# Performance work log

Measured on AMD Instinct MI355X. Metric: run time of the kernel, lower is better.

## Reference

```python
import jax, jax.numpy as jnp
import numpy as np

DIM = 768
N_HEADS = 12
HEAD_DIM = DIM // N_HEADS
SCALE = HEAD_DIM ** -0.5


def setup_inputs() -> dict:
    key = jax.random.key(0)
    ks = jax.random.split(key, 5)
    B, N = 8, 1024
    x = jax.random.normal(ks[0], (B, N, DIM), dtype=jnp.float32)
    # Linear weights stored as (in, out) for x @ W; torch stores (out, in).
    w_qkv = jax.random.normal(ks[1], (DIM, 3 * DIM), dtype=jnp.float32) * (DIM ** -0.5)
    b_qkv = jnp.zeros((3 * DIM,), dtype=jnp.float32)
    w_proj = jax.random.normal(ks[2], (DIM, DIM), dtype=jnp.float32) * (DIM ** -0.5)
    b_proj = jnp.zeros((DIM,), dtype=jnp.float32)
    return {"x": x, "w_qkv": w_qkv, "b_qkv": b_qkv, "w_proj": w_proj, "b_proj": b_proj}


def reference(x, w_qkv, b_qkv, w_proj, b_proj):
    B, N, _ = x.shape
    qkv = x @ w_qkv + b_qkv                       # [B, N, 3*dim]
    qkv = qkv.reshape(B, N, 3, N_HEADS, HEAD_DIM)
    qkv = jnp.transpose(qkv, (2, 0, 3, 1, 4))     # [3, B, H, N, hd]
    q, k, v = qkv[0], qkv[1], qkv[2]
    attn = jnp.einsum("bhqd,bhkd->bhqk", q, k) * SCALE
    attn = jax.nn.softmax(attn, axis=-1)
    out = jnp.einsum("bhqk,bhkd->bhqd", attn, v)  # [B, H, N, hd]
    out = jnp.transpose(out, (0, 2, 1, 3)).reshape(B, N, DIM)
    return out @ w_proj + b_proj
```

## Files before the change

### kernel.cpp

```cpp
#include <hip/hip_runtime.h>
#include <cstdint>

#define DIM 768
#define NH 12
#define HD 64
#define SEQ 1024
#define NBH 96

#define QOFF  ((size_t)0)
#define KOFF  ((size_t)6291456)
#define VOFF  ((size_t)12582912)
#define AOFF  ((size_t)18874368)
#define XOFF  ((size_t)25165824)
#define WQOFF ((size_t)31457280)
#define WPOFF ((size_t)33226752)

#define QSCALE 0.18033688f

#define WAIT_VM0   __builtin_amdgcn_s_waitcnt(0x0F70)
#define BAR        __builtin_amdgcn_s_barrier()
#define CFENCE     __asm__ __volatile__("" ::: "memory")

typedef __attribute__((ext_vector_type(8))) __bf16 bf16x8;
typedef __attribute__((ext_vector_type(2))) __bf16 bf16x2;
typedef __attribute__((ext_vector_type(4))) float f32x4;
typedef __attribute__((ext_vector_type(4))) short s16x4;
typedef unsigned short u16;

__device__ __forceinline__ u16 f2bf(float f) {
    union { float f; unsigned u; } x; x.f = f;
    unsigned r = x.u + 0x7fffu + ((x.u >> 16) & 1u);
    return (u16)(r >> 16);
}

__device__ __forceinline__ unsigned pkbf(float a, float b) {
#if __has_builtin(__builtin_amdgcn_cvt_pk_bf16_f32)
    bf16x2 v = __builtin_amdgcn_cvt_pk_bf16_f32(a, b);
    union { bf16x2 v; unsigned u; } c; c.v = v; return c.u;
#else
    return (unsigned)f2bf(a) | ((unsigned)f2bf(b) << 16);
#endif
}

__device__ __forceinline__ void async_cp16(const void* g, void* l) {
    __builtin_amdgcn_global_load_lds((const __attribute__((address_space(1))) void*)g,
                                     (__attribute__((address_space(3))) void*)l, 16, 0, 0);
}

__global__ __launch_bounds__(256) void prep(const float* __restrict__ x,
                                            const float* __restrict__ wq,
                                            const float* __restrict__ wp,
                                            u16* __restrict__ ws) {
    const int bid = blockIdx.x;
    const int tid = threadIdx.x;
    if (bid < 3072) {
        size_t i = (size_t)bid * 512 + tid;
#pragma unroll
        for (int j = 0; j < 2; ++j, i += 256) {
            float4 v = *(const float4*)&x[i * 4];
            ushort4 o;
            o.x = f2bf(v.x); o.y = f2bf(v.y); o.z = f2bf(v.z); o.w = f2bf(v.w);
            *(ushort4*)&ws[XOFF + i * 4] = o;
        }
        return;
    }
    __shared__ float T[64][65];
    const float* w; u16* wt; int N, bx, by;
    if (bid < 3504) { int b = bid - 3072; w = wq; wt = ws + WQOFF; N = 2304; bx = b % 36; by = b / 36; }
    else            { int b = bid - 3504; w = wp; wt = ws + WPOFF; N = 768;  bx = b % 12; by = b / 12; }
    const int K = 768;
    const int k0 = by * 64, n0 = bx * 64;
    const int r = tid >> 4, c4 = (tid & 15) * 4;
#pragma unroll
    for (int i = 0; i < 4; ++i) {
        float4 v = *(const float4*)&w[(size_t)(k0 + r + 16 * i) * N + n0 + c4];
        T[r + 16 * i][c4 + 0] = v.x; T[r + 16 * i][c4 + 1] = v.y;
        T[r + 16 * i][c4 + 2] = v.z; T[r + 16 * i][c4 + 3] = v.w;
    }
    __syncthreads();
#pragma unroll
    for (int i = 0; i < 4; ++i) {
        int rr = r + 16 * i;
        ushort4 o;
        o.x = f2bf(T[c4 + 0][rr]); o.y = f2bf(T[c4 + 1][rr]);
        o.z = f2bf(T[c4 + 2][rr]); o.w = f2bf(T[c4 + 3][rr]);
        *(ushort4*)&wt[(size_t)(n0 + rr) * K + k0 + c4] = o;
    }
}

template <int EPI, int NC>
__global__ __launch_bounds__(256, 3) void gemm_bt(const u16* __restrict__ A,
                                                  const u16* __restrict__ Bt,
                                                  const float* __restrict__ bias,
                                                  float* __restrict__ outf,
                                                  u16* __restrict__ outq) {
    __shared__ __align__(16) u16 As[128 * 64];
    __shared__ __align__(16) u16 Bs[32 * NC * 64];
    const int tid = threadIdx.x;
    const int lane = tid & 63;
    const int w = tid >> 6;
    const int wm = w >> 1, wn = w & 1;
    const int m0 = blockIdx.y * 128, n0 = blockIdx.x * (32 * NC);

    const int lgrp = lane >> 3;
    const int gg = (lane & 7) ^ lgrp;
    const u16* ga = A  + (size_t)(m0 + w * 32 + lgrp) * 768 + gg * 8;
    const u16* gb = Bt + (size_t)(n0 + w * 8 * NC + lgrp) * 768 + gg * 8;
    u16* lba = As + w * 32 * 64;
    u16* lbb = Bs + w * 8 * NC * 64;

    const int l15 = lane & 15, qg = lane >> 4, q4 = qg * 4;

    int aoff[4][2], boff[NC][2];
#pragma unroll
    for (int r = 0; r < 4; ++r) {
        int row = 64 * wm + 16 * r + l15;
#pragma unroll
        for (int kc = 0; kc < 2; ++kc)
            aoff[r][kc] = row * 64 + (((4 * kc + qg) ^ (row & 7)) << 3);
    }
#pragma unroll
    for (int c = 0; c < NC; ++c) {
        int row = 16 * NC * wn + 16 * c + l15;
#pragma unroll
        for (int kc = 0; kc < 2; ++kc)
            boff[c][kc] = row * 64 + (((4 * kc + qg) ^ (row & 7)) << 3);
    }

    f32x4 acc[4][NC] = {};

    for (int k0 = 0; k0 < 768; k0 += 64) {
#pragma unroll
        for (int i = 0; i < 4; ++i)
            async_cp16(ga + (size_t)i * 8 * 768 + k0, lba + i * 512);
#pragma unroll
        for (int i = 0; i < NC; ++i)
            async_cp16(gb + (size_t)i * 8 * 768 + k0, lbb + i * 512);
        __syncthreads();
#pragma unroll
        for (int kc = 0; kc < 2; ++kc) {
            bf16x8 af[4], bfr[NC];
#pragma unroll
            for (int r = 0; r < 4; ++r) af[r] = *(const bf16x8*)&As[aoff[r][kc]];
#pragma unroll
            for (int c = 0; c < NC; ++c) bfr[c] = *(const bf16x8*)&Bs[boff[c][kc]];
#pragma unroll
            for (int r = 0; r < 4; ++r)
#pragma unroll
                for (int c = 0; c < NC; ++c)
                    acc[r][c] = __builtin_amdgcn_mfma_f32_16x16x32_bf16(af[r], bfr[c], acc[r][c], 0, 0, 0);
        }
        __syncthreads();
    }

#pragma unroll
    for (int r = 0; r < 4; ++r) {
#pragma unroll
        for (int c = 0; c < NC; ++c) {
            const int cg = n0 + 16 * NC * wn + 16 * c + l15;
            const float bv = bias[cg];
            const int mb = m0 + 64 * wm + 16 * r + q4;
            if constexpr (EPI == 0) {
#pragma unroll
                for (int g = 0; g < 4; ++g)
                    outf[(size_t)(mb + g) * DIM + cg] = acc[r][c][g] + bv;
            } else {
                const int which = (cg >= 1536) ? 2 : (cg >= 768 ? 1 : 0);
                const int rem = cg - which * 768;
                const int h = rem >> 6, d = rem & 63;
                const int b = mb >> 10, q = mb & 1023;
                if (which == 0) {
#pragma unroll
                    for (int g = 0; g < 4; ++g)
                        outq[QOFF + ((size_t)(b * NH + h) * SEQ + q + g) * HD + d] =
                            f2bf((acc[r][c][g] + bv) * QSCALE);
                } else if (which == 1) {
#pragma unroll
                    for (int g = 0; g < 4; ++g)
                        outq[KOFF + ((size_t)(b * NH + h) * SEQ + q + g) * HD + d] =
                            f2bf(acc[r][c][g] + bv);
                } else {
                    ushort4 pk;
                    pk.x = f2bf(acc[r][c][0] + bv); pk.y = f2bf(acc[r][c][1] + bv);
                    pk.z = f2bf(acc[r][c][2] + bv); pk.w = f2bf(acc[r][c][3] + bv);
                    *(ushort4*)&outq[VOFF + ((size_t)(b * NH + h) * HD + d) * SEQ + q] = pk;
                }
            }
        }
    }
}

__global__ __launch_bounds__(256) void flash_attn(const u16* __restrict__ ws, u16* __restrict__ attn_out) {
    __shared__ __align__(16) u16 Ks[2][64 * 64];
    __shared__ __align__(16) u16 Vs[2][64 * 64];

    const int tid = threadIdx.x;
    const int lane = tid & 63;
    const int wv = tid >> 6;
    const int qt = blockIdx.x;
    const int bh = blockIdx.y;
    const u16* qp = ws + QOFF + (size_t)bh * SEQ * HD;
    const u16* kp = ws + KOFF + (size_t)bh * SEQ * HD;
    const u16* vp = ws + VOFF + (size_t)bh * HD * SEQ;

    const int l15 = lane & 15, qg = lane >> 4, q8 = qg * 8;
    const int l7 = l15 & 7;

    bf16x8 bq[2][2];
#pragma unroll
    for (int r = 0; r < 2; ++r)
#pragma unroll
        for (int kc = 0; kc < 2; ++kc)
            bq[r][kc] = *(const bf16x8*)&qp[(size_t)(qt * 128 + 32 * wv + 16 * r + l15) * HD + 32 * kc + q8];

    const int lgrp = lane >> 3;
    const int gg = (lane & 7) ^ lgrp;
    auto stage = [&](int buf, int ktv) {
#pragma unroll
        for (int i = 0; i < 2; ++i) {
            async_cp16(kp + (size_t)(ktv * 64 + wv * 16 + i * 8 + lgrp) * 64 + gg * 8,
                       &Ks[buf][(wv * 16 + i * 8) * 64]);
            async_cp16(vp + (size_t)(wv * 16 + i * 8 + lgrp) * SEQ + ktv * 64 + gg * 8,
                       &Vs[buf][(wv * 16 + i * 8) * 64]);
        }
    };
    stage(0, 0);

    int akoff[4][2], avoff[4][4];
#pragma unroll
    for (int c = 0; c < 4; ++c) {
#pragma unroll
        for (int kc = 0; kc < 2; ++kc)
            akoff[c][kc] = (16 * c + l15) * 64 + (((4 * kc + qg) ^ l7) << 3);
#pragma unroll
        for (int cd = 0; cd < 4; ++cd)
            avoff[c][cd] = (16 * cd + l15) * 64 + (((2 * c + (qg >> 1)) ^ l7) << 3) + (qg & 1) * 4;
    }

    f32x4 oacc[2][4] = {};
    float lsum[2] = {0.f, 0.f};

    for (int kt = 0; kt < 16; ++kt) {
        const int cur = kt & 1;
        WAIT_VM0;
        BAR;
        CFENCE;
        if (kt < 15) stage(cur ^ 1, kt + 1);

        f32x4 sacc[4][2] = {};
#pragma unroll
        for (int c = 0; c < 4; ++c) {
#pragma unroll
            for (int kc = 0; kc < 2; ++kc) {
                bf16x8 ak = *(const bf16x8*)&Ks[cur][akoff[c][kc]];
#pragma unroll
                for (int r = 0; r < 2; ++r)
                    sacc[c][r] = __builtin_amdgcn_mfma_f32_16x16x32_bf16(ak, bq[r][kc], sacc[c][r], 0, 0, 0);
            }
        }

        s16x4 pf[4][2];
#pragma unroll
        for (int c = 0; c < 4; ++c) {
#pragma unroll
            for (int r = 0; r < 2; ++r) {
                float p0 = __builtin_amdgcn_exp2f(sacc[c][r][0]);
                float p1 = __builtin_amdgcn_exp2f(sacc[c][r][1]);
                float p2 = __builtin_amdgcn_exp2f(sacc[c][r][2]);
                float p3 = __builtin_amdgcn_exp2f(sacc[c][r][3]);
                lsum[r] += (p0 + p1) + (p2 + p3);
                union { uint2 u; s16x4 v; } pk;
                pk.u.x = pkbf(p0, p1); pk.u.y = pkbf(p2, p3);
                pf[c][r] = pk.v;
            }
        }

#pragma unroll
        for (int c = 0; c < 4; ++c) {
            s16x4 av[4];
#pragma unroll
            for (int cd = 0; cd < 4; ++cd)
                av[cd] = *(const s16x4*)&Vs[cur][avoff[c][cd]];
#pragma unroll
            for (int r = 0; r < 2; ++r)
#pragma unroll
                for (int cd = 0; cd < 4; ++cd)
                    oacc[r][cd] = __builtin_amdgcn_mfma_f32_16x16x16bf16_1k(av[cd], pf[c][r], oacc[r][cd], 0, 0, 0);
        }
    }

#pragma unroll
    for (int r = 0; r < 2; ++r) {
        lsum[r] += __shfl_xor(lsum[r], 16);
        lsum[r] += __shfl_xor(lsum[r], 32);
    }

    const int b = bh / NH, h = bh % NH;
#pragma unroll
    for (int r = 0; r < 2; ++r) {
        const float inv = 1.f / lsum[r];
        const int qrow = qt * 128 + 32 * wv + 16 * r + l15;
        u16* orow = attn_out + (size_t)(b * SEQ + qrow) * DIM + h * HD + qg * 4;
#pragma unroll
        for (int cd = 0; cd < 4; ++cd) {
            ushort4 o;
            o.x = f2bf(oacc[r][cd][0] * inv); o.y = f2bf(oacc[r][cd][1] * inv);
            o.z = f2bf(oacc[r][cd][2] * inv); o.w = f2bf(oacc[r][cd][3] * inv);
            *(ushort4*)&orow[16 * cd] = o;
        }
    }
}

extern "C" void kernel_launch(void* const* d_in, const int* in_sizes, int n_in,
                              void* d_out, int out_size, void* d_ws, size_t ws_size,
                              hipStream_t stream) {
    const float* x      = (const float*)d_in[0];
    const float* w_qkv  = (const float*)d_in[1];
    const float* b_qkv  = (const float*)d_in[2];
    const float* w_proj = (const float*)d_in[3];
    const float* b_proj = (const float*)d_in[4];
    float* out = (float*)d_out;
    u16* ws = (u16*)d_ws;

    prep<<<3648, 256, 0, stream>>>(x, w_qkv, w_proj, ws);
    gemm_bt<1, 4><<<dim3(18, 64), 256, 0, stream>>>(ws + XOFF, ws + WQOFF, b_qkv, nullptr, ws);
    flash_attn<<<dim3(8, 96), 256, 0, stream>>>(ws, ws + AOFF);
    gemm_bt<0, 2><<<dim3(12, 64), 256, 0, stream>>>(ws + AOFF, ws + WPOFF, b_proj, out, nullptr);
}
```

Before: 195.4 us.

## Pipeline GEMM with 4-stage async LDS buffers, 128x128 tiles, XCD-aware block remap

Rewrites the bf16 GEMM kernel to use 512-thread blocks with 128x128 output tiles and a four-buffer LDS ring. Global-to-LDS async copies run three k-steps ahead, with partial vmcnt waits and a single barrier per step instead of two. Block indices are remapped so consecutive tiles land on the same XCD for L2 reuse, and MFMA sections are given raised priority with s_setprio. The change uses 128KB of LDS per block, which limits occupancy to one block per CU. The projection GEMM grid shrinks to 384 blocks, which may underfill the GPU.

Result: slower. 209.6 us (+7.3%).

```diff
diff --git a/kernel.cpp b/kernel.cpp
--- a/kernel.cpp
+++ b/kernel.cpp
@@ -18,6 +18,7 @@
 #define QSCALE 0.18033688f
 
 #define WAIT_VM0   __builtin_amdgcn_s_waitcnt(0x0F70)
+#define WAIT_VM(n) __builtin_amdgcn_s_waitcnt(0x0F70 | (n))
 #define BAR        __builtin_amdgcn_s_barrier()
 #define CFENCE     __asm__ __volatile__("" ::: "memory")
 
@@ -88,30 +89,35 @@
     }
 }
 
-template <int EPI, int NC>
-__global__ __launch_bounds__(256, 3) void gemm_bt(const u16* __restrict__ A,
+template <int EPI>
+__global__ __launch_bounds__(512, 2) void gemm_bt(const u16* __restrict__ A,
                                                   const u16* __restrict__ Bt,
                                                   const float* __restrict__ bias,
                                                   float* __restrict__ outf,
                                                   u16* __restrict__ outq) {
-    __shared__ __align__(16) u16 As[128 * 64];
-    __shared__ __align__(16) u16 Bs[32 * NC * 64];
+    constexpr int NT = 12;
+    __shared__ __align__(16) u16 As[4][128 * 64];
+    __shared__ __align__(16) u16 Bs[4][128 * 64];
     const int tid = threadIdx.x;
     const int lane = tid & 63;
     const int w = tid >> 6;
-    const int wm = w >> 1, wn = w & 1;
-    const int m0 = blockIdx.y * 128, n0 = blockIdx.x * (32 * NC);
+    const int wm = w >> 2, wn = w & 3;
+
+    const int gx = gridDim.x;
+    const int flat = blockIdx.y * gx + blockIdx.x;
+    const int chunk = (gx * gridDim.y) >> 3;
+    const int nf = (flat & 7) * chunk + (flat >> 3);
+    const int bxs = nf % gx, bys = nf / gx;
+    const int m0 = bys * 128, n0 = bxs * 128;
 
     const int lgrp = lane >> 3;
     const int gg = (lane & 7) ^ lgrp;
-    const u16* ga = A  + (size_t)(m0 + w * 32 + lgrp) * 768 + gg * 8;
-    const u16* gb = Bt + (size_t)(n0 + w * 8 * NC + lgrp) * 768 + gg * 8;
-    u16* lba = As + w * 32 * 64;
-    u16* lbb = Bs + w * 8 * NC * 64;
+    const u16* ga = A  + (size_t)(m0 + w * 16 + lgrp) * 768 + gg * 8;
+    const u16* gb = Bt + (size_t)(n0 + w * 16 + lgrp) * 768 + gg * 8;
 
     const int l15 = lane & 15, qg = lane >> 4, q4 = qg * 4;
 
-    int aoff[4][2], boff[NC][2];
+    int aoff[4][2], boff[2][2];
 #pragma unroll
     for (int r = 0; r < 4; ++r) {
         int row = 64 * wm + 16 * r + l15;
@@ -120,44 +126,61 @@
             aoff[r][kc] = row * 64 + (((4 * kc + qg) ^ (row & 7)) << 3);
     }
 #pragma unroll
-    for (int c = 0; c < NC; ++c) {
-        int row = 16 * NC * wn + 16 * c + l15;
+    for (int c = 0; c < 2; ++c) {
+        int row = 32 * wn + 16 * c + l15;
 #pragma unroll
         for (int kc = 0; kc < 2; ++kc)
             boff[c][kc] = row * 64 + (((4 * kc + qg) ^ (row & 7)) << 3);
     }
 
-    f32x4 acc[4][NC] = {};
-
-    for (int k0 = 0; k0 < 768; k0 += 64) {
-#pragma unroll
-        for (int i = 0; i < 4; ++i)
-            async_cp16(ga + (size_t)i * 8 * 768 + k0, lba + i * 512);
-#pragma unroll
-        for (int i = 0; i < NC; ++i)
-            async_cp16(gb + (size_t)i * 8 * 768 + k0, lbb + i * 512);
-        __syncthreads();
+    f32x4 acc[4][2] = {};
+
+    auto stageT = [&](int t) {
+        const int buf = t & 3;
+        const size_t ko = (size_t)t * 64;
+#pragma unroll
+        for (int i = 0; i < 2; ++i) {
+            async_cp16(ga + (size_t)i * 8 * 768 + ko, &As[buf][(w * 16 + i * 8) * 64]);
+            async_cp16(gb + (size_t)i * 8 * 768 + ko, &Bs[buf][(w * 16 + i * 8) * 64]);
+        }
+    };
+    auto compute = [&](int buf) {
 #pragma unroll
         for (int kc = 0; kc < 2; ++kc) {
-            bf16x8 af[4], bfr[NC];
-#pragma unroll
-            for (int r = 0; r < 4; ++r) af[r] = *(const bf16x8*)&As[aoff[r][kc]];
-#pragma unroll
-            for (int c = 0; c < NC; ++c) bfr[c] = *(const bf16x8*)&Bs[boff[c][kc]];
+            bf16x8 af[4], bfr[2];
+#pragma unroll
+            for (int r = 0; r < 4; ++r) af[r] = *(const bf16x8*)&As[buf][aoff[r][kc]];
+#pragma unroll
+            for (int c = 0; c < 2; ++c) bfr[c] = *(const bf16x8*)&Bs[buf][boff[c][kc]];
+            __builtin_amdgcn_s_setprio(1);
 #pragma unroll
             for (int r = 0; r < 4; ++r)
 #pragma unroll
-                for (int c = 0; c < NC; ++c)
+                for (int c = 0; c < 2; ++c)
                     acc[r][c] = __builtin_amdgcn_mfma_f32_16x16x32_bf16(af[r], bfr[c], acc[r][c], 0, 0, 0);
-        }
-        __syncthreads();
-    }
+            __builtin_amdgcn_s_setprio(0);
+        }
+    };
+
+    stageT(0); stageT(1); stageT(2);
+
+    int t = 0;
+    for (; t < NT - 3; ++t) {
+        WAIT_VM(8);
+        BAR;
+        CFENCE;
+        stageT(t + 3);
+        compute(t & 3);
+    }
+    WAIT_VM(8); BAR; CFENCE; compute(t & 3); ++t;
+    WAIT_VM(4); BAR; CFENCE; compute(t & 3); ++t;
+    WAIT_VM0;   BAR; CFENCE; compute(t & 3);
 
 #pragma unroll
     for (int r = 0; r < 4; ++r) {
 #pragma unroll
-        for (int c = 0; c < NC; ++c) {
-            const int cg = n0 + 16 * NC * wn + 16 * c + l15;
+        for (int c = 0; c < 2; ++c) {
+            const int cg = n0 + 32 * wn + 16 * c + l15;
             const float bv = bias[cg];
             const int mb = m0 + 64 * wm + 16 * r + q4;
             if constexpr (EPI == 0) {
@@ -323,7 +346,7 @@
     u16* ws = (u16*)d_ws;
 
     prep<<<3648, 256, 0, stream>>>(x, w_qkv, w_proj, ws);
-    gemm_bt<1, 4><<<dim3(18, 64), 256, 0, stream>>>(ws + XOFF, ws + WQOFF, b_qkv, nullptr, ws);
+    gemm_bt<1><<<dim3(18, 64), 512, 0, stream>>>(ws + XOFF, ws + WQOFF, b_qkv, nullptr, ws);
     flash_attn<<<dim3(8, 96), 256, 0, stream>>>(ws, ws + AOFF);
-    gemm_bt<0, 2><<<dim3(12, 64), 256, 0, stream>>>(ws + AOFF, ws + WPOFF, b_proj, out, nullptr);
-}
+    gemm_bt<0><<<dim3(6, 64), 512, 0, stream>>>(ws + AOFF, ws + WPOFF, b_proj, out, nullptr);
+}
```
